# Performance work log

Hardware: AMD Instinct MI355X
Metric: run time of the kernel (lower is better)

The kernel has to match this reference:

```python
import jax, jax.numpy as jnp
import numpy as np

N = 50000        # num nodes
E = 1_000_000    # num edges
F_IN = 256       # input feature dim
UNITS = 128      # hidden units
NUM_CLASSES = 40 # output classes
EPS = 1e-3       # Keras BatchNormalization default epsilon


def setup_inputs() -> dict:
    key = jax.random.key(0)
    ks = jax.random.split(key, 32)
    inp = {
        "x": jax.random.normal(ks[0], (N, F_IN), jnp.float32),
        "edge_index": jax.random.randint(ks[1], (2, E), 0, N, jnp.int32),
        "edge_weight": jax.random.uniform(ks[2], (E,), jnp.float32),
    }
    dims = [(F_IN, UNITS), (UNITS, UNITS), (UNITS, NUM_CLASSES)]
    ki = 3
    for li, (fi, fo) in enumerate(dims, 1):
        inp[f"w_gcn{li}"] = jax.random.normal(ks[ki], (fi, fo), jnp.float32) / np.sqrt(fi).astype(np.float32); ki += 1
        inp[f"w_self{li}"] = jax.random.normal(ks[ki], (fi, fo), jnp.float32) / np.sqrt(fi).astype(np.float32); ki += 1
        inp[f"b{li}"] = jnp.zeros((fo,), jnp.float32)
        inp[f"gamma{li}"] = 1.0 + 0.1 * jax.random.normal(ks[ki], (fo,), jnp.float32); ki += 1
        inp[f"beta{li}"] = 0.1 * jax.random.normal(ks[ki], (fo,), jnp.float32); ki += 1
        inp[f"mean{li}"] = 0.1 * jax.random.normal(ks[ki], (fo,), jnp.float32); ki += 1
        inp[f"var{li}"] = jnp.ones((fo,), jnp.float32)
    return inp


def _gcn_bs(h, src, dst, norm_w, w_gcn, w_self, b, gamma, beta, mean, var, act):
    # GCN aggregation: transform then gather->weight->scatter-sum
    hw = h @ w_gcn                                   # [N, out]
    msg = hw[src] * norm_w[:, None]                  # [E, out]
    agg = jax.ops.segment_sum(msg, dst, num_segments=N)
    out = agg + h @ w_self + b                       # self-loop dense + bias
    # BatchNorm (inference: moving stats)
    out = (out - mean) * jax.lax.rsqrt(var + EPS) * gamma + beta
    return act(out) if act is not None else out


def reference(x, edge_index, edge_weight,
              w_gcn1, w_self1, b1, gamma1, beta1, mean1, var1,
              w_gcn2, w_self2, b2, gamma2, beta2, mean2, var2,
              w_gcn3, w_self3, b3, gamma3, beta3, mean3, var3):
    src, dst = edge_index[0], edge_index[1]
    # symmetric GCN normalization (renorm=False: no added self loops)
    deg = jax.ops.segment_sum(edge_weight, dst, num_segments=N)
    dinv = jnp.where(deg > 0, jax.lax.rsqrt(jnp.where(deg > 0, deg, 1.0)), 0.0)
    norm_w = dinv[src] * edge_weight * dinv[dst]
    # inference: DropEdge and Dropout are identity
    h = _gcn_bs(x, src, dst, norm_w, w_gcn1, w_self1, b1, gamma1, beta1, mean1, var1, jax.nn.relu)
    h = _gcn_bs(h, src, dst, norm_w, w_gcn2, w_self2, b2, gamma2, beta2, mean2, var2, jax.nn.relu)
    h = _gcn_bs(h, src, dst, norm_w, w_gcn3, w_self3, b3, gamma3, beta3, mean3, var3, None)
    return h
```

## Files before the change

### kernel.cpp

```cpp
#include <hip/hip_runtime.h>
#include <hip/hip_bf16.h>

#define NN 50000
#define EE 1000000
static constexpr float EPSV = 1e-3f;
static constexpr float FIXSCALE = 16777216.f;

typedef __attribute__((ext_vector_type(8))) short short8;
typedef __attribute__((ext_vector_type(4))) float fx4;

__device__ inline float blo(unsigned u) { return __uint_as_float(u << 16); }
__device__ inline float bhi(unsigned u) { return __uint_as_float(u & 0xffff0000u); }
__device__ inline unsigned short f2b(float f) {
    __hip_bfloat16 h = __float2bfloat16(f);
    return *(unsigned short*)&h;
}
__device__ inline unsigned pack2(float a, float b) {
    return (unsigned)f2b(a) | ((unsigned)f2b(b) << 16);
}

__device__ inline void gload_lds16(const unsigned short* g, unsigned short* ldsbase) {
    __builtin_amdgcn_global_load_lds(
        (const __attribute__((address_space(1))) unsigned int*)(const void*)g,
        (__attribute__((address_space(3))) unsigned int*)(void*)ldsbase, 16, 0, 0);
}


#define ZB 196
#define WB1 256
#define WB2 128
#define WB3 64
#define XB 12500

__global__ void setupx_kernel(unsigned long long* __restrict__ cnt64p,
                              const float* __restrict__ wg1, const float* __restrict__ ws1,
                              unsigned short* __restrict__ Wt1,
                              const float* __restrict__ wg2, const float* __restrict__ ws2,
                              unsigned short* __restrict__ Wt2,
                              const float* __restrict__ wg3, const float* __restrict__ ws3,
                              unsigned short* __restrict__ Wt3,
                              const float4* __restrict__ x, uint2* __restrict__ xb) {
    int b = blockIdx.x;
    int t = threadIdx.x;
    if (b < ZB) {
        int i = b * 256 + t;
        if (i < NN) cnt64p[(size_t)i << 3] = 0ull;
    } else if (b < ZB + WB1) {
        int idx = (b - ZB) * 256 + t;
        int n = idx >> 8, k = idx & 255;
        float v = (n < 128) ? wg1[(size_t)k * 128 + n]
                            : ws1[(size_t)k * 128 + (n - 128)];
        Wt1[idx] = f2b(v);
    } else if (b < ZB + WB1 + WB2) {
        int idx = (b - ZB - WB1) * 256 + t;
        int n = idx >> 7, k = idx & 127;
        float v = (n < 128) ? wg2[(size_t)k * 128 + n]
                            : ws2[(size_t)k * 128 + (n - 128)];
        Wt2[idx] = f2b(v);
    } else if (b < ZB + WB1 + WB2 + WB3) {
        int idx = (b - ZB - WB1 - WB2) * 256 + t;
        int n = idx >> 7, k = idx & 127;
        float v = 0.f;
        if (n < 40) v = wg3[(size_t)k * 40 + n];
        else if (n < 80) v = ws3[(size_t)k * 40 + (n - 40)];
        Wt3[idx] = f2b(v);
    } else {
        int i = (b - ZB - WB1 - WB2 - WB3) * 256 + t;
        float4 v = x[i];
        xb[i] = make_uint2(pack2(v.x, v.y), pack2(v.z, v.w));
    }
}


__device__ __forceinline__ void gemm2ph_body(int bx, int by,
                                             const unsigned short* __restrict__ Ab,
                                             const unsigned short* __restrict__ Wt,
                                             const float* __restrict__ bias,
                                             unsigned short* __restrict__ Cg,
                                             unsigned short* __restrict__ Cs,
                                             int M, int K, int Fo,
                                             unsigned short* sA, unsigned short* sB) {
    const int t = threadIdx.x;
    const int lane = t & 63;
    const int wave = t >> 6;
    const int l15 = lane & 15, quad = lane >> 4;
    const int row0 = bx * 64;
    const int colbase = by * 128;

    fx4 acc[4][2];
#pragma unroll
    for (int r = 0; r < 4; ++r)
#pragma unroll
        for (int c = 0; c < 2; ++c) acc[r][c] = (fx4){0.f, 0.f, 0.f, 0.f};

    auto stage = [&](int kc, int half) {
        unsigned short* dA = sA + half * 2048;
        unsigned short* dB = sB + half * 4096;
#pragma unroll
        for (int j = 0; j < 3; ++j) {
            int o = wave * 3 + j;
            int ak = kc + quad * 8;
            if (o < 4) {
                int ar = row0 + o * 16 + l15;
                if (ar >= M) ar = M - 1;
                gload_lds16(Ab + (size_t)ar * K + ak, dA + o * 512);
            } else {
                int bo = o - 4;
                int br = colbase + bo * 16 + l15;
                gload_lds16(Wt + (size_t)br * K + ak, dB + bo * 512);
            }
        }
    };

    stage(0, 0);
    __syncthreads();
    const int nt = K >> 5;
    int cur = 0;
    for (int tt = 0; tt < nt; ++tt) {
        if (tt + 1 < nt) stage((tt + 1) * 32, cur ^ 1);
        const unsigned short* cA = sA + cur * 2048;
        const unsigned short* cB = sB + cur * 4096;
        short8 a[4], b[2];
#pragma unroll
        for (int r = 0; r < 4; ++r)
            a[r] = *reinterpret_cast<const short8*>(&cA[r * 512 + lane * 8]);
#pragma unroll
        for (int c = 0; c < 2; ++c)
            b[c] = *reinterpret_cast<const short8*>(&cB[(wave * 2 + c) * 512 + lane * 8]);
#pragma unroll
        for (int r = 0; r < 4; ++r)
#pragma unroll
            for (int c = 0; c < 2; ++c)
                acc[r][c] = __builtin_amdgcn_mfma_f32_16x16x32_bf16(a[r], b[c], acc[r][c], 0, 0, 0);
        __syncthreads();
        cur ^= 1;
    }

#pragma unroll
    for (int r = 0; r < 4; ++r) {
#pragma unroll
        for (int reg = 0; reg < 4; ++reg) {
            int row = row0 + r * 16 + quad * 4 + reg;
            if (row >= M) continue;
#pragma unroll
            for (int c = 0; c < 2; ++c) {
                int f = colbase + wave * 32 + c * 16 + l15;
                if (f >= 2 * Fo) continue;
                bool isG = (f < Fo);
                int col = isG ? f : f - Fo;
                float badd = isG ? 0.f : bias[col];
                unsigned short* basep = isG ? Cg : Cs;
                basep[(size_t)row * Fo + col] = f2b(acc[r][c][reg] + badd);
            }
        }
    }
}


#define AB 256
#define GX 782
#define GB 1564

__global__ __launch_bounds__(256) void mega_kernel(
    const int* __restrict__ ei, const float* __restrict__ ew,
    unsigned long long* __restrict__ cnt64p, unsigned* __restrict__ rank,
    const unsigned short* __restrict__ xb, const unsigned short* __restrict__ Wt1,
    const float* __restrict__ bias1,
    unsigned short* __restrict__ Cg, unsigned short* __restrict__ Cs) {
    __shared__ unsigned short sA[2 * 64 * 32];
    __shared__ unsigned short sB[2 * 128 * 32];
    int b = blockIdx.x;
    if (b < AB) {
        int gtid = b * 256 + threadIdx.x;
#pragma unroll
        for (int g = 0; g < 2; ++g) {
            int d[8];
            unsigned fx[8];
            bool val[8];
#pragma unroll
            for (int j = 0; j < 8; ++j) {
                int e = (g * 8 + j) * 65536 + gtid;
                val[j] = (e < EE);
                if (val[j]) {
                    d[j] = ei[EE + e];
                    fx[j] = __float2uint_rn(ew[e] * FIXSCALE);
                }
            }
#pragma unroll
            for (int j = 0; j < 8; ++j) {
                if (val[j]) {
                    int e = (g * 8 + j) * 65536 + gtid;
                    unsigned long long old =
                        atomicAdd(&cnt64p[(size_t)d[j] << 3],
                                  0x100000000ull | (unsigned long long)fx[j]);
                    rank[e] = (unsigned)(old >> 32);
                }
            }
        }
        return;
    }
    int gi = b - AB;
    int by = gi / GX;
    int bx = gi - by * GX;
    gemm2ph_body(bx, by, xb, Wt1, bias1, Cg, Cs, NN, 256, 128, sA, sB);
}


__global__ __launch_bounds__(1024) void dinvsum_kernel(const unsigned long long* __restrict__ cnt64p,
                                                       float* __restrict__ dinv,
                                                       int* __restrict__ bsum) {
    __shared__ int s[1024];
    const int t = threadIdx.x;
    int idx = blockIdx.x * 1024 + t;
    unsigned long long cv = 0ull;
    if (idx < NN) cv = cnt64p[(size_t)idx << 3];
    float deg = (float)(unsigned)cv * (1.f / FIXSCALE);
    if (idx < NN) dinv[idx] = (deg > 0.f) ? rsqrtf(deg) : 0.f;
    s[t] = (int)(unsigned)(cv >> 32);
    __syncthreads();
#pragma unroll
    for (int off = 512; off > 0; off >>= 1) {
        if (t < off) s[t] += s[t + off];
        __syncthreads();
    }
    if (t == 0) bsum[blockIdx.x] = s[0];
}

__global__ __launch_bounds__(64) void scanB_kernel(const int* __restrict__ bsum,
                                                   int* __restrict__ bpre, int nb) {
    int t = threadIdx.x;
    int v = (t < nb) ? bsum[t] : 0;
    int own = v;
#pragma unroll
    for (int off = 1; off < 64; off <<= 1) {
        int u = __shfl_up(v, off);
        if (t >= off) v += u;
    }
    if (t < nb) bpre[t] = v - own;
}

__global__ __launch_bounds__(1024) void scanC_kernel(const unsigned long long* __restrict__ cnt64p,
                                                     const int* __restrict__ bpre,
                                                     int* __restrict__ rowstart) {
    __shared__ int s[1024];
    const int t = threadIdx.x;
    int idx = blockIdx.x * 1024 + t;
    int v = (idx < NN) ? (int)(unsigned)(cnt64p[(size_t)idx << 3] >> 32) : 0;
    s[t] = v;
    __syncthreads();
#pragma unroll
    for (int off = 1; off < 1024; off <<= 1) {
        int u = (t >= off) ? s[t - off] : 0;
        __syncthreads();
        s[t] += u;
        __syncthreads();
    }
    if (idx < NN) rowstart[idx] = s[t] - v + bpre[blockIdx.x];
    if (idx == 0) rowstart[NN] = EE;
}

__global__ void fill_kernel(const int* __restrict__ ei, const float* __restrict__ ew,
                            const float* __restrict__ dinv, const int* __restrict__ rowstart,
                            const unsigned* __restrict__ rank, unsigned* __restrict__ eprec4) {
    int e = blockIdx.x * blockDim.x + threadIdx.x;
    if (e >= EE) return;
    int s = ei[e], d = ei[EE + e];
    int idx = rowstart[d] + (int)rank[e];
    float w = dinv[s] * ew[e] * dinv[d];
    eprec4[idx] = ((unsigned)s << 16) | (unsigned)f2b(w);
}

__global__ __launch_bounds__(256) void gemm_mfma(const unsigned short* __restrict__ Ab,
                                                 const unsigned short* __restrict__ Wt,
                                                 const float* __restrict__ bias,
                                                 unsigned short* __restrict__ Cg,
                                                 unsigned short* __restrict__ Cs,
                                                 int M, int K, int Fo) {
    __shared__ unsigned short sA[2 * 64 * 32];
    __shared__ unsigned short sB[2 * 128 * 32];
    gemm2ph_body(blockIdx.x, blockIdx.y, Ab, Wt, bias, Cg, Cs, M, K, Fo, sA, sB);
}


template <bool RELU>
__global__ __launch_bounds__(256) void agg128_kernel(
    const int* __restrict__ rowstart, const unsigned* __restrict__ eprec4,
    const unsigned* __restrict__ hw, const unsigned* __restrict__ selfC,
    const float* __restrict__ g, const float* __restrict__ be,
    const float* __restrict__ mu, const float* __restrict__ va,
    unsigned* __restrict__ out) {
    int wave = threadIdx.x >> 6;
    int lane = threadIdx.x & 63;
    int n = blockIdx.x * 4 + wave;
    if (n >= NN) return;
    unsigned scp = selfC[n * 64 + lane];
    float acc0 = blo(scp), acc1 = bhi(scp);
    int beg = rowstart[n], end = rowstart[n + 1];
    int i = beg;

    if (i + 16 <= end) {
        unsigned e[16];
        {
            int ifl = __builtin_amdgcn_readfirstlane(i);
#pragma unroll
            for (int k = 0; k < 16; ++k) e[k] = eprec4[ifl + k];
        }
        for (; i + 32 <= end; i += 16) {
            unsigned v[16];
#pragma unroll
            for (int k = 0; k < 16; ++k) v[k] = hw[(e[k] >> 16) * 64u + lane];
            unsigned en[16];
            {
                int ifl = __builtin_amdgcn_readfirstlane(i + 16);
#pragma unroll
                for (int k = 0; k < 16; ++k) en[k] = eprec4[ifl + k];
            }
#pragma unroll
            for (int k = 0; k < 16; ++k) {
                float w = blo(e[k]);
                acc0 += blo(v[k]) * w;
                acc1 += bhi(v[k]) * w;
            }
#pragma unroll
            for (int k = 0; k < 16; ++k) e[k] = en[k];
        }
        unsigned v[16];
#pragma unroll
        for (int k = 0; k < 16; ++k) v[k] = hw[(e[k] >> 16) * 64u + lane];
#pragma unroll
        for (int k = 0; k < 16; ++k) {
            float w = blo(e[k]);
            acc0 += blo(v[k]) * w;
            acc1 += bhi(v[k]) * w;
        }
        i += 16;
    }
    for (; i + 4 <= end; i += 4) {
        unsigned e0 = eprec4[i], e1 = eprec4[i + 1], e2 = eprec4[i + 2], e3 = eprec4[i + 3];
        unsigned v0 = hw[(e0 >> 16) * 64u + lane];
        unsigned v1 = hw[(e1 >> 16) * 64u + lane];
        unsigned v2 = hw[(e2 >> 16) * 64u + lane];
        unsigned v3 = hw[(e3 >> 16) * 64u + lane];
        float w0 = blo(e0), w1 = blo(e1), w2 = blo(e2), w3 = blo(e3);
        acc0 += blo(v0) * w0; acc1 += bhi(v0) * w0;
        acc0 += blo(v1) * w1; acc1 += bhi(v1) * w1;
        acc0 += blo(v2) * w2; acc1 += bhi(v2) * w2;
        acc0 += blo(v3) * w3; acc1 += bhi(v3) * w3;
    }
    for (; i < end; ++i) {
        unsigned e = eprec4[i];
        unsigned v = hw[(e >> 16) * 64u + lane];
        float w = blo(e);
        acc0 += blo(v) * w; acc1 += bhi(v) * w;
    }
    float2 m2 = reinterpret_cast<const float2*>(mu)[lane];
    float2 v2f = reinterpret_cast<const float2*>(va)[lane];
    float2 g2 = reinterpret_cast<const float2*>(g)[lane];
    float2 b2 = reinterpret_cast<const float2*>(be)[lane];
    float r0 = (acc0 - m2.x) * rsqrtf(v2f.x + EPSV) * g2.x + b2.x;
    float r1 = (acc1 - m2.y) * rsqrtf(v2f.y + EPSV) * g2.y + b2.y;
    if (RELU) {
        r0 = fmaxf(r0, 0.f);
        r1 = fmaxf(r1, 0.f);
    }
    out[n * 64 + lane] = pack2(r0, r1);
}


__global__ __launch_bounds__(256) void agg40_kernel(
    const int* __restrict__ rowstart, const unsigned* __restrict__ eprec4,
    const unsigned* __restrict__ hw, const unsigned* __restrict__ selfC,
    const float* __restrict__ g, const float* __restrict__ be,
    const float* __restrict__ mu, const float* __restrict__ va,
    float* __restrict__ out) {
    int wave = threadIdx.x >> 6;
    int lane = threadIdx.x & 63;
    int n = blockIdx.x * 4 + wave;
    if (n >= NN) return;
    int grp = lane / 20;
    int fl = lane - grp * 20;
    float acc0 = 0.f, acc1 = 0.f;
    int beg = rowstart[n], end = rowstart[n + 1];
    if (grp < 3) {
        int i = beg + grp;
        for (; i + 9 < end; i += 12) {
            unsigned e0 = eprec4[i], e1 = eprec4[i + 3], e2 = eprec4[i + 6], e3 = eprec4[i + 9];
            unsigned v0 = hw[(e0 >> 16) * 20u + fl];
            unsigned v1 = hw[(e1 >> 16) * 20u + fl];
            unsigned v2 = hw[(e2 >> 16) * 20u + fl];
            unsigned v3 = hw[(e3 >> 16) * 20u + fl];
            float w0 = blo(e0), w1 = blo(e1), w2 = blo(e2), w3 = blo(e3);
            acc0 += blo(v0) * w0; acc1 += bhi(v0) * w0;
            acc0 += blo(v1) * w1; acc1 += bhi(v1) * w1;
            acc0 += blo(v2) * w2; acc1 += bhi(v2) * w2;
            acc0 += blo(v3) * w3; acc1 += bhi(v3) * w3;
        }
        for (; i < end; i += 3) {
            unsigned e = eprec4[i];
            unsigned v = hw[(e >> 16) * 20u + fl];
            float w = blo(e);
            acc0 += blo(v) * w;
            acc1 += bhi(v) * w;
        }
    }
    acc0 += __shfl(acc0, lane + 20) + __shfl(acc0, lane + 40);
    acc1 += __shfl(acc1, lane + 20) + __shfl(acc1, lane + 40);
    if (lane < 20) {
        int f0 = lane * 2;
        unsigned scp = selfC[n * 20 + lane];
        acc0 += blo(scp);
        acc1 += bhi(scp);
        float2 m2 = reinterpret_cast<const float2*>(mu)[lane];
        float2 v2f = reinterpret_cast<const float2*>(va)[lane];
        float2 g2 = reinterpret_cast<const float2*>(g)[lane];
        float2 b2 = reinterpret_cast<const float2*>(be)[lane];
        float r0 = (acc0 - m2.x) * rsqrtf(v2f.x + EPSV) * g2.x + b2.x;
        float r1 = (acc1 - m2.y) * rsqrtf(v2f.y + EPSV) * g2.y + b2.y;
        *reinterpret_cast<float2*>(&out[(size_t)n * 40 + f0]) = make_float2(r0, r1);
    }
}


extern "C" void kernel_launch(void* const* d_in, const int* in_sizes, int n_in,
                              void* d_out, int out_size, void* d_ws, size_t ws_size,
                              hipStream_t stream) {
    const float* x = (const float*)d_in[0];
    const int* ei = (const int*)d_in[1];
    const float* ew = (const float*)d_in[2];

    const float* wg[3]  = {(const float*)d_in[3],  (const float*)d_in[10], (const float*)d_in[17]};
    const float* wsf[3] = {(const float*)d_in[4],  (const float*)d_in[11], (const float*)d_in[18]};
    const float* bs[3]  = {(const float*)d_in[5],  (const float*)d_in[12], (const float*)d_in[19]};
    const float* gm[3]  = {(const float*)d_in[6],  (const float*)d_in[13], (const float*)d_in[20]};
    const float* bt[3]  = {(const float*)d_in[7],  (const float*)d_in[14], (const float*)d_in[21]};
    const float* mu[3]  = {(const float*)d_in[8],  (const float*)d_in[15], (const float*)d_in[22]};
    const float* vr[3]  = {(const float*)d_in[9],  (const float*)d_in[16], (const float*)d_in[23]};

    float* W = (float*)d_ws;
    float* dinv     = W + 100096;
    unsigned* rank  = (unsigned*)(W + 150144);
    int*   bsum     = (int*)(W + 1150144);
    int*   bpre     = (int*)(W + 1150208);
    int*   rowstart = (int*)(W + 1150272);
    unsigned* eprec4 = (unsigned*)(W + 1200384);
    unsigned short* Wt1 = (unsigned short*)(W + 2200384);
    unsigned short* Wt2 = (unsigned short*)(W + 2233152);
    unsigned short* Wt3 = (unsigned short*)(W + 2249536);
    unsigned short* xb  = (unsigned short*)(W + 2257728);
    unsigned short* bufH = (unsigned short*)(W + 2257728);
    unsigned short* bufHW = (unsigned short*)(W + 8657728);
    unsigned short* bufSb = (unsigned short*)(W + 11857728);
    unsigned long long* cnt64p = (unsigned long long*)(W + 15057728);

    const int B = 256;
    const int SB = 49;

    setupx_kernel<<<ZB + WB1 + WB2 + WB3 + XB, B, 0, stream>>>(
        cnt64p, wg[0], wsf[0], Wt1, wg[1], wsf[1], Wt2, wg[2], wsf[2], Wt3,
        (const float4*)x, (uint2*)xb);

    mega_kernel<<<AB + GB, B, 0, stream>>>(ei, ew, cnt64p, rank, xb, Wt1, bs[0],
                                           bufHW, bufSb);

    dinvsum_kernel<<<SB, 1024, 0, stream>>>(cnt64p, dinv, bsum);
    scanB_kernel<<<1, 64, 0, stream>>>(bsum, bpre, SB);
    scanC_kernel<<<SB, 1024, 0, stream>>>(cnt64p, bpre, rowstart);
    fill_kernel<<<(EE + B - 1) / B, B, 0, stream>>>(ei, ew, dinv, rowstart, rank, eprec4);

    const int aggGrid = (NN + 3) / 4;
    dim3 g2(GX, 2), g1(GX, 1);

    agg128_kernel<true><<<aggGrid, B, 0, stream>>>(rowstart, eprec4, (const unsigned*)bufHW,
                                                   (const unsigned*)bufSb, gm[0], bt[0], mu[0], vr[0],
                                                   (unsigned*)bufH);

    gemm_mfma<<<g2, B, 0, stream>>>(bufH, Wt2, bs[1], bufHW, bufSb, NN, 128, 128);
    agg128_kernel<true><<<aggGrid, B, 0, stream>>>(rowstart, eprec4, (const unsigned*)bufHW,
                                                   (const unsigned*)bufSb, gm[1], bt[1], mu[1], vr[1],
                                                   (unsigned*)bufH);

    gemm_mfma<<<g1, B, 0, stream>>>(bufH, Wt3, bs[2], bufHW, bufSb, NN, 128, 40);
    agg40_kernel<<<aggGrid, B, 0, stream>>>(rowstart, eprec4, (const unsigned*)bufHW,
                                            (const unsigned*)bufSb, gm[2], bt[2], mu[2], vr[2],
                                            (float*)d_out);
}
```

Before: 379.6 us.

## Fuse layer aggregation with the next layer's MFMA GEMM

Each 256-thread block now aggregates 16 nodes (one wave per four nodes), applies BatchNorm and ReLU, and stages the bf16 results in LDS. The same block then multiplies them by the next layer's concatenated gcn/self weights with 16x16x32 bf16 MFMA and writes both outputs directly. This removes two standalone GEMM launches and the global round trip of the intermediate hidden tensor. In exchange the blocks are larger, the weights are read per block straight from global memory rather than tiled, and the MFMA phase waits on a barrier behind the slowest aggregating wave.

```diff
diff --git a/kernel.cpp b/kernel.cpp
--- a/kernel.cpp
+++ b/kernel.cpp
@@ -270,100 +270,122 @@
     eprec4[idx] = ((unsigned)s << 16) | (unsigned)f2b(w);
 }
 
-__global__ __launch_bounds__(256) void gemm_mfma(const unsigned short* __restrict__ Ab,
-                                                 const unsigned short* __restrict__ Wt,
-                                                 const float* __restrict__ bias,
-                                                 unsigned short* __restrict__ Cg,
-                                                 unsigned short* __restrict__ Cs,
-                                                 int M, int K, int Fo) {
-    __shared__ unsigned short sA[2 * 64 * 32];
-    __shared__ unsigned short sB[2 * 128 * 32];
-    gemm2ph_body(blockIdx.x, blockIdx.y, Ab, Wt, bias, Cg, Cs, M, K, Fo, sA, sB);
-}
-
-
-template <bool RELU>
-__global__ __launch_bounds__(256) void agg128_kernel(
+
+template <int FO, int CTW>
+__global__ __launch_bounds__(256) void aggemm_kernel(
     const int* __restrict__ rowstart, const unsigned* __restrict__ eprec4,
     const unsigned* __restrict__ hw, const unsigned* __restrict__ selfC,
     const float* __restrict__ g, const float* __restrict__ be,
     const float* __restrict__ mu, const float* __restrict__ va,
-    unsigned* __restrict__ out) {
-    int wave = threadIdx.x >> 6;
-    int lane = threadIdx.x & 63;
-    int n = blockIdx.x * 4 + wave;
-    if (n >= NN) return;
-    unsigned scp = selfC[n * 64 + lane];
-    float acc0 = blo(scp), acc1 = bhi(scp);
-    int beg = rowstart[n], end = rowstart[n + 1];
-    int i = beg;
-
-    if (i + 16 <= end) {
-        unsigned e[16];
-        {
-            int ifl = __builtin_amdgcn_readfirstlane(i);
-#pragma unroll
-            for (int k = 0; k < 16; ++k) e[k] = eprec4[ifl + k];
-        }
-        for (; i + 32 <= end; i += 16) {
+    const unsigned short* __restrict__ Wt, const float* __restrict__ bias,
+    unsigned short* __restrict__ Cg, unsigned short* __restrict__ Cs) {
+    __shared__ unsigned short sh[16 * 144];
+    const int wave = threadIdx.x >> 6;
+    const int lane = threadIdx.x & 63;
+    const int l15 = lane & 15, quad = lane >> 4;
+    const int n0 = blockIdx.x * 16;
+
+    for (int j = 0; j < 4; ++j) {
+        int nd = wave * 4 + j;
+        int n = n0 + nd;
+        unsigned scp = selfC[n * 64 + lane];
+        float acc0 = blo(scp), acc1 = bhi(scp);
+        int beg = rowstart[n], end = rowstart[n + 1];
+        int i = beg;
+        if (i + 16 <= end) {
+            unsigned e[16];
+            {
+                int ifl = __builtin_amdgcn_readfirstlane(i);
+#pragma unroll
+                for (int k = 0; k < 16; ++k) e[k] = eprec4[ifl + k];
+            }
+            for (; i + 32 <= end; i += 16) {
+                unsigned v[16];
+#pragma unroll
+                for (int k = 0; k < 16; ++k) v[k] = hw[(e[k] >> 16) * 64u + lane];
+                unsigned en[16];
+                {
+                    int ifl = __builtin_amdgcn_readfirstlane(i + 16);
+#pragma unroll
+                    for (int k = 0; k < 16; ++k) en[k] = eprec4[ifl + k];
+                }
+#pragma unroll
+                for (int k = 0; k < 16; ++k) {
+                    float w = blo(e[k]);
+                    acc0 += blo(v[k]) * w;
+                    acc1 += bhi(v[k]) * w;
+                }
+#pragma unroll
+                for (int k = 0; k < 16; ++k) e[k] = en[k];
+            }
             unsigned v[16];
 #pragma unroll
             for (int k = 0; k < 16; ++k) v[k] = hw[(e[k] >> 16) * 64u + lane];
-            unsigned en[16];
-            {
-                int ifl = __builtin_amdgcn_readfirstlane(i + 16);
-#pragma unroll
-                for (int k = 0; k < 16; ++k) en[k] = eprec4[ifl + k];
-            }
 #pragma unroll
             for (int k = 0; k < 16; ++k) {
                 float w = blo(e[k]);
                 acc0 += blo(v[k]) * w;
                 acc1 += bhi(v[k]) * w;
             }
-#pragma unroll
-            for (int k = 0; k < 16; ++k) e[k] = en[k];
-        }
-        unsigned v[16];
-#pragma unroll
-        for (int k = 0; k < 16; ++k) v[k] = hw[(e[k] >> 16) * 64u + lane];
-#pragma unroll
-        for (int k = 0; k < 16; ++k) {
-            float w = blo(e[k]);
-            acc0 += blo(v[k]) * w;
-            acc1 += bhi(v[k]) * w;
-        }
-        i += 16;
-    }
-    for (; i + 4 <= end; i += 4) {
-        unsigned e0 = eprec4[i], e1 = eprec4[i + 1], e2 = eprec4[i + 2], e3 = eprec4[i + 3];
-        unsigned v0 = hw[(e0 >> 16) * 64u + lane];
-        unsigned v1 = hw[(e1 >> 16) * 64u + lane];
-        unsigned v2 = hw[(e2 >> 16) * 64u + lane];
-        unsigned v3 = hw[(e3 >> 16) * 64u + lane];
-        float w0 = blo(e0), w1 = blo(e1), w2 = blo(e2), w3 = blo(e3);
-        acc0 += blo(v0) * w0; acc1 += bhi(v0) * w0;
-        acc0 += blo(v1) * w1; acc1 += bhi(v1) * w1;
-        acc0 += blo(v2) * w2; acc1 += bhi(v2) * w2;
-        acc0 += blo(v3) * w3; acc1 += bhi(v3) * w3;
-    }
-    for (; i < end; ++i) {
-        unsigned e = eprec4[i];
-        unsigned v = hw[(e >> 16) * 64u + lane];
-        float w = blo(e);
-        acc0 += blo(v) * w; acc1 += bhi(v) * w;
-    }
-    float2 m2 = reinterpret_cast<const float2*>(mu)[lane];
-    float2 v2f = reinterpret_cast<const float2*>(va)[lane];
-    float2 g2 = reinterpret_cast<const float2*>(g)[lane];
-    float2 b2 = reinterpret_cast<const float2*>(be)[lane];
-    float r0 = (acc0 - m2.x) * rsqrtf(v2f.x + EPSV) * g2.x + b2.x;
-    float r1 = (acc1 - m2.y) * rsqrtf(v2f.y + EPSV) * g2.y + b2.y;
-    if (RELU) {
+            i += 16;
+        }
+        for (; i + 4 <= end; i += 4) {
+            unsigned e0 = eprec4[i], e1 = eprec4[i + 1], e2 = eprec4[i + 2], e3 = eprec4[i + 3];
+            unsigned v0 = hw[(e0 >> 16) * 64u + lane];
+            unsigned v1 = hw[(e1 >> 16) * 64u + lane];
+            unsigned v2 = hw[(e2 >> 16) * 64u + lane];
+            unsigned v3 = hw[(e3 >> 16) * 64u + lane];
+            float w0 = blo(e0), w1 = blo(e1), w2 = blo(e2), w3 = blo(e3);
+            acc0 += blo(v0) * w0; acc1 += bhi(v0) * w0;
+            acc0 += blo(v1) * w1; acc1 += bhi(v1) * w1;
+            acc0 += blo(v2) * w2; acc1 += bhi(v2) * w2;
+            acc0 += blo(v3) * w3; acc1 += bhi(v3) * w3;
+        }
+        for (; i < end; ++i) {
+            unsigned e = eprec4[i];
+            unsigned v = hw[(e >> 16) * 64u + lane];
+            float w = blo(e);
+            acc0 += blo(v) * w; acc1 += bhi(v) * w;
+        }
+        float2 m2 = reinterpret_cast<const float2*>(mu)[lane];
+        float2 v2f = reinterpret_cast<const float2*>(va)[lane];
+        float2 g2 = reinterpret_cast<const float2*>(g)[lane];
+        float2 b2 = reinterpret_cast<const float2*>(be)[lane];
+        float r0 = (acc0 - m2.x) * rsqrtf(v2f.x + EPSV) * g2.x + b2.x;
+        float r1 = (acc1 - m2.y) * rsqrtf(v2f.y + EPSV) * g2.y + b2.y;
         r0 = fmaxf(r0, 0.f);
         r1 = fmaxf(r1, 0.f);
-    }
-    out[n * 64 + lane] = pack2(r0, r1);
+        *reinterpret_cast<unsigned*>(reinterpret_cast<char*>(sh) + nd * 288 + lane * 4) =
+            pack2(r0, r1);
+    }
+    __syncthreads();
+
+    short8 af[4];
+#pragma unroll
+    for (int ks = 0; ks < 4; ++ks)
+        af[ks] = *reinterpret_cast<const short8*>(
+            reinterpret_cast<const char*>(sh) + l15 * 288 + ks * 64 + quad * 16);
+#pragma unroll
+    for (int ct = 0; ct < CTW; ++ct) {
+        int colf = (wave * CTW + ct) * 16 + l15;
+        fx4 acc = (fx4){0.f, 0.f, 0.f, 0.f};
+#pragma unroll
+        for (int ks = 0; ks < 4; ++ks) {
+            short8 bf = *reinterpret_cast<const short8*>(Wt + (size_t)colf * 128 + ks * 32 + quad * 8);
+            acc = __builtin_amdgcn_mfma_f32_16x16x32_bf16(af[ks], bf, acc, 0, 0, 0);
+        }
+        if (colf < 2 * FO) {
+            bool isG = (colf < FO);
+            int col = isG ? colf : colf - FO;
+            float badd = isG ? 0.f : bias[col];
+            unsigned short* basep = isG ? Cg : Cs;
+#pragma unroll
+            for (int reg = 0; reg < 4; ++reg) {
+                int row = n0 + quad * 4 + reg;
+                basep[(size_t)row * FO + col] = f2b(acc[reg] + badd);
+            }
+        }
+    }
 }
 
 
@@ -447,7 +469,8 @@
     unsigned short* Wt2 = (unsigned short*)(W + 2233152);
     unsigned short* Wt3 = (unsigned short*)(W + 2249536);
     unsigned short* xb  = (unsigned short*)(W + 2257728);
-    unsigned short* bufH = (unsigned short*)(W + 2257728);
+    unsigned short* bufHW2 = (unsigned short*)(W + 2257728);
+    unsigned short* bufSb2 = (unsigned short*)(W + 5457728);
     unsigned short* bufHW = (unsigned short*)(W + 8657728);
     unsigned short* bufSb = (unsigned short*)(W + 11857728);
     unsigned long long* cnt64p = (unsigned long long*)(W + 15057728);
@@ -467,20 +490,15 @@
     scanC_kernel<<<SB, 1024, 0, stream>>>(cnt64p, bpre, rowstart);
     fill_kernel<<<(EE + B - 1) / B, B, 0, stream>>>(ei, ew, dinv, rowstart, rank, eprec4);
 
-    const int aggGrid = (NN + 3) / 4;
-    dim3 g2(GX, 2), g1(GX, 1);
-
-    agg128_kernel<true><<<aggGrid, B, 0, stream>>>(rowstart, eprec4, (const unsigned*)bufHW,
-                                                   (const unsigned*)bufSb, gm[0], bt[0], mu[0], vr[0],
-                                                   (unsigned*)bufH);
-
-    gemm_mfma<<<g2, B, 0, stream>>>(bufH, Wt2, bs[1], bufHW, bufSb, NN, 128, 128);
-    agg128_kernel<true><<<aggGrid, B, 0, stream>>>(rowstart, eprec4, (const unsigned*)bufHW,
-                                                   (const unsigned*)bufSb, gm[1], bt[1], mu[1], vr[1],
-                                                   (unsigned*)bufH);
-
-    gemm_mfma<<<g1, B, 0, stream>>>(bufH, Wt3, bs[2], bufHW, bufSb, NN, 128, 40);
-    agg40_kernel<<<aggGrid, B, 0, stream>>>(rowstart, eprec4, (const unsigned*)bufHW,
-                                            (const unsigned*)bufSb, gm[2], bt[2], mu[2], vr[2],
-                                            (float*)d_out);
-}
+    aggemm_kernel<128, 4><<<NN / 16, B, 0, stream>>>(
+        rowstart, eprec4, (const unsigned*)bufHW, (const unsigned*)bufSb,
+        gm[0], bt[0], mu[0], vr[0], Wt2, bs[1], bufHW2, bufSb2);
+
+    aggemm_kernel<40, 2><<<NN / 16, B, 0, stream>>>(
+        rowstart, eprec4, (const unsigned*)bufHW2, (const unsigned*)bufSb2,
+        gm[1], bt[1], mu[1], vr[1], Wt3, bs[2], bufHW, bufSb);
+
+    agg40_kernel<<<(NN + 3) / 4, B, 0, stream>>>(rowstart, eprec4, (const unsigned*)bufHW,
+                                                 (const unsigned*)bufSb, gm[2], bt[2], mu[2], vr[2],
+                                                 (float*)d_out);
+}
```

Result: slower. 396.4 us (+4.4%).

## Replace 64-bit fixed-point degree atomics with count-only atomics and CSR-side degree reduction

Applied to the files above, without the earlier changes.

The edge-count atomic no longer packs a fixed-point edge-weight sum into a 64-bit word; it becomes a 32-bit count increment. Weighted degree is instead computed after the CSR fill by a per-node wave reduction over a temporary weight array, and a second pass rescales each edge record with the normalized weight. This aims to cut atomic width and drop the float-to-fixed conversion. It also removes fixed-point rounding in the degree. In exchange it adds two kernels and extra scattered memory traffic over the edge array.

```diff
diff --git a/kernel.cpp b/kernel.cpp
--- a/kernel.cpp
+++ b/kernel.cpp
@@ -4,7 +4,6 @@
 #define NN 50000
 #define EE 1000000
 static constexpr float EPSV = 1e-3f;
-static constexpr float FIXSCALE = 16777216.f;
 
 typedef __attribute__((ext_vector_type(8))) short short8;
 typedef __attribute__((ext_vector_type(4))) float fx4;
@@ -32,7 +31,7 @@
 #define WB3 64
 #define XB 12500
 
-__global__ void setupx_kernel(unsigned long long* __restrict__ cnt64p,
+__global__ void setupx_kernel(unsigned* __restrict__ cnt32p,
                               const float* __restrict__ wg1, const float* __restrict__ ws1,
                               unsigned short* __restrict__ Wt1,
                               const float* __restrict__ wg2, const float* __restrict__ ws2,
@@ -44,7 +43,7 @@
     int t = threadIdx.x;
     if (b < ZB) {
         int i = b * 256 + t;
-        if (i < NN) cnt64p[(size_t)i << 3] = 0ull;
+        if (i < NN) cnt32p[(size_t)i << 4] = 0u;
     } else if (b < ZB + WB1) {
         int idx = (b - ZB) * 256 + t;
         int n = idx >> 8, k = idx & 255;
@@ -162,8 +161,8 @@
 #define GB 1564
 
 __global__ __launch_bounds__(256) void mega_kernel(
-    const int* __restrict__ ei, const float* __restrict__ ew,
-    unsigned long long* __restrict__ cnt64p, unsigned* __restrict__ rank,
+    const int* __restrict__ ei,
+    unsigned* __restrict__ cnt32p, unsigned* __restrict__ rank,
     const unsigned short* __restrict__ xb, const unsigned short* __restrict__ Wt1,
     const float* __restrict__ bias1,
     unsigned short* __restrict__ Cg, unsigned short* __restrict__ Cs) {
@@ -175,25 +174,18 @@
 #pragma unroll
         for (int g = 0; g < 2; ++g) {
             int d[8];
-            unsigned fx[8];
             bool val[8];
 #pragma unroll
             for (int j = 0; j < 8; ++j) {
                 int e = (g * 8 + j) * 65536 + gtid;
                 val[j] = (e < EE);
-                if (val[j]) {
-                    d[j] = ei[EE + e];
-                    fx[j] = __float2uint_rn(ew[e] * FIXSCALE);
-                }
+                if (val[j]) d[j] = ei[EE + e];
             }
 #pragma unroll
             for (int j = 0; j < 8; ++j) {
                 if (val[j]) {
                     int e = (g * 8 + j) * 65536 + gtid;
-                    unsigned long long old =
-                        atomicAdd(&cnt64p[(size_t)d[j] << 3],
-                                  0x100000000ull | (unsigned long long)fx[j]);
-                    rank[e] = (unsigned)(old >> 32);
+                    rank[e] = atomicAdd(&cnt32p[(size_t)d[j] << 4], 1u);
                 }
             }
         }
@@ -206,17 +198,12 @@
 }
 
 
-__global__ __launch_bounds__(1024) void dinvsum_kernel(const unsigned long long* __restrict__ cnt64p,
-                                                       float* __restrict__ dinv,
-                                                       int* __restrict__ bsum) {
+__global__ __launch_bounds__(1024) void cntsum_kernel(const unsigned* __restrict__ cnt32p,
+                                                      int* __restrict__ bsum) {
     __shared__ int s[1024];
     const int t = threadIdx.x;
     int idx = blockIdx.x * 1024 + t;
-    unsigned long long cv = 0ull;
-    if (idx < NN) cv = cnt64p[(size_t)idx << 3];
-    float deg = (float)(unsigned)cv * (1.f / FIXSCALE);
-    if (idx < NN) dinv[idx] = (deg > 0.f) ? rsqrtf(deg) : 0.f;
-    s[t] = (int)(unsigned)(cv >> 32);
+    s[t] = (idx < NN) ? (int)cnt32p[(size_t)idx << 4] : 0;
     __syncthreads();
 #pragma unroll
     for (int off = 512; off > 0; off >>= 1) {
@@ -239,13 +226,13 @@
     if (t < nb) bpre[t] = v - own;
 }
 
-__global__ __launch_bounds__(1024) void scanC_kernel(const unsigned long long* __restrict__ cnt64p,
+__global__ __launch_bounds__(1024) void scanC_kernel(const unsigned* __restrict__ cnt32p,
                                                      const int* __restrict__ bpre,
                                                      int* __restrict__ rowstart) {
     __shared__ int s[1024];
     const int t = threadIdx.x;
     int idx = blockIdx.x * 1024 + t;
-    int v = (idx < NN) ? (int)(unsigned)(cnt64p[(size_t)idx << 3] >> 32) : 0;
+    int v = (idx < NN) ? (int)cnt32p[(size_t)idx << 4] : 0;
     s[t] = v;
     __syncthreads();
 #pragma unroll
@@ -260,14 +247,45 @@
 }
 
 __global__ void fill_kernel(const int* __restrict__ ei, const float* __restrict__ ew,
-                            const float* __restrict__ dinv, const int* __restrict__ rowstart,
-                            const unsigned* __restrict__ rank, unsigned* __restrict__ eprec4) {
+                            const int* __restrict__ rowstart,
+                            const unsigned* __restrict__ rank,
+                            unsigned* __restrict__ eprec4, float* __restrict__ wtmp) {
     int e = blockIdx.x * blockDim.x + threadIdx.x;
     if (e >= EE) return;
     int s = ei[e], d = ei[EE + e];
     int idx = rowstart[d] + (int)rank[e];
-    float w = dinv[s] * ew[e] * dinv[d];
-    eprec4[idx] = ((unsigned)s << 16) | (unsigned)f2b(w);
+    eprec4[idx] = (unsigned)s << 16;
+    wtmp[idx] = ew[e];
+}
+
+__global__ __launch_bounds__(256) void dinvw_kernel(const int* __restrict__ rowstart,
+                                                    const float* __restrict__ wtmp,
+                                                    float* __restrict__ dinv) {
+    int wave = threadIdx.x >> 6, lane = threadIdx.x & 63;
+    int n = blockIdx.x * 4 + wave;
+    if (n >= NN) return;
+    int beg = rowstart[n], end = rowstart[n + 1];
+    float a = 0.f;
+    for (int i = beg + lane; i < end; i += 64) a += wtmp[i];
+#pragma unroll
+    for (int off = 32; off > 0; off >>= 1) a += __shfl_xor(a, off);
+    if (lane == 0) dinv[n] = (a > 0.f) ? rsqrtf(a) : 0.f;
+}
+
+__global__ __launch_bounds__(256) void rescale_kernel(const int* __restrict__ rowstart,
+                                                      const float* __restrict__ wtmp,
+                                                      const float* __restrict__ dinv,
+                                                      unsigned* __restrict__ eprec4) {
+    int wave = threadIdx.x >> 6, lane = threadIdx.x & 63;
+    int n = blockIdx.x * 4 + wave;
+    if (n >= NN) return;
+    float dn = dinv[n];
+    int beg = rowstart[n], end = rowstart[n + 1];
+    for (int i = beg + lane; i < end; i += 64) {
+        unsigned rec = eprec4[i];
+        float w = wtmp[i] * dinv[rec >> 16] * dn;
+        eprec4[i] = (rec & 0xffff0000u) | (unsigned)f2b(w);
+    }
 }
 
 __global__ __launch_bounds__(256) void gemm_mfma(const unsigned short* __restrict__ Ab,
@@ -447,25 +465,28 @@
     unsigned short* Wt2 = (unsigned short*)(W + 2233152);
     unsigned short* Wt3 = (unsigned short*)(W + 2249536);
     unsigned short* xb  = (unsigned short*)(W + 2257728);
+    float* wtmp     = W + 2257728;
     unsigned short* bufH = (unsigned short*)(W + 2257728);
     unsigned short* bufHW = (unsigned short*)(W + 8657728);
     unsigned short* bufSb = (unsigned short*)(W + 11857728);
-    unsigned long long* cnt64p = (unsigned long long*)(W + 15057728);
+    unsigned* cnt32p = (unsigned*)(W + 15057728);
 
     const int B = 256;
     const int SB = 49;
 
     setupx_kernel<<<ZB + WB1 + WB2 + WB3 + XB, B, 0, stream>>>(
-        cnt64p, wg[0], wsf[0], Wt1, wg[1], wsf[1], Wt2, wg[2], wsf[2], Wt3,
+        cnt32p, wg[0], wsf[0], Wt1, wg[1], wsf[1], Wt2, wg[2], wsf[2], Wt3,
         (const float4*)x, (uint2*)xb);
 
-    mega_kernel<<<AB + GB, B, 0, stream>>>(ei, ew, cnt64p, rank, xb, Wt1, bs[0],
+    mega_kernel<<<AB + GB, B, 0, stream>>>(ei, cnt32p, rank, xb, Wt1, bs[0],
                                            bufHW, bufSb);
 
-    dinvsum_kernel<<<SB, 1024, 0, stream>>>(cnt64p, dinv, bsum);
+    cntsum_kernel<<<SB, 1024, 0, stream>>>(cnt32p, bsum);
     scanB_kernel<<<1, 64, 0, stream>>>(bsum, bpre, SB);
-    scanC_kernel<<<SB, 1024, 0, stream>>>(cnt64p, bpre, rowstart);
-    fill_kernel<<<(EE + B - 1) / B, B, 0, stream>>>(ei, ew, dinv, rowstart, rank, eprec4);
+    scanC_kernel<<<SB, 1024, 0, stream>>>(cnt32p, bpre, rowstart);
+    fill_kernel<<<(EE + B - 1) / B, B, 0, stream>>>(ei, ew, rowstart, rank, eprec4, wtmp);
+    dinvw_kernel<<<(NN + 3) / 4, B, 0, stream>>>(rowstart, wtmp, dinv);
+    rescale_kernel<<<(NN + 3) / 4, B, 0, stream>>>(rowstart, wtmp, dinv, eprec4);
 
     const int aggGrid = (NN + 3) / 4;
     dim3 g2(GX, 2), g1(GX, 1);
```

Result: slower. 402.6 us (+6.0%).
